# Optimization experiments

Measured on AMD Instinct MI355X. Metric: run time of the kernel, lower is better.

## Reference

```python
import jax, jax.numpy as jnp
import numpy as np


def setup_inputs() -> dict:
    key = jax.random.key(0)
    ks = jax.random.split(key, 9)
    N, K, CS, CT, OUT, S = 50000, 16, 64, 64, 64, 4
    x = jax.random.normal(ks[0], (N, CT), dtype=jnp.float32)
    src = jax.random.normal(ks[1], (N, CS), dtype=jnp.float32)
    neighbor_idx = jax.random.randint(ks[2], (N, K), 0, N, dtype=jnp.int32)
    scale_t = 1.0 / np.sqrt(CT)
    scale_s = 1.0 / np.sqrt(CS)
    Wt = jax.random.normal(ks[3], (CT, S), dtype=jnp.float32) * scale_t
    bt = jax.random.normal(ks[4], (S,), dtype=jnp.float32) * scale_t
    Ws = jax.random.normal(ks[5], (CS, S), dtype=jnp.float32) * scale_s
    bs = jax.random.normal(ks[6], (S,), dtype=jnp.float32) * scale_s
    W_lin = jax.random.normal(ks[7], (S, CS, OUT), dtype=jnp.float32) * scale_s
    b_lin = jax.random.normal(ks[8], (S, OUT), dtype=jnp.float32) * scale_s
    return {"x": x, "src": src, "neighbor_idx": neighbor_idx,
            "Wt": Wt, "bt": bt, "Ws": Ws, "bs": bs,
            "W_lin": W_lin, "b_lin": b_lin}


def reference(x, src, neighbor_idx, Wt, bt, Ws, bs, W_lin, b_lin):
    # Gather per-node neighbor messages: [N, K, Cs]
    msgs = src[neighbor_idx]
    size = Wt.shape[-1]
    # target assignment logits from own data: [N, S]
    t = x @ Wt + bt
    # source assignment logits from messages: [N, K, S]
    s = jnp.einsum('nkc,cs->nks', msgs, Ws) + bs
    # soft assignment over the `size` weight matrices (softmax over S)
    a = jax.nn.softmax(s + t[:, None, :], axis=-1)  # [N, K, S]
    # apply each of the `size` linears to the messages: [N, K, S, O]
    w = jnp.einsum('nkc,sco->nkso', msgs, W_lin) + b_lin
    # assignment-weighted mean over the S weight matrices: [N, K, O]
    out = jnp.einsum('nks,nkso->nko', a, w) / size
    return out
```

## Files before the change

kernel.cpp:

```cpp
#include <hip/hip_runtime.h>

#define CT 64
#define CS 64
#define K_NB 16
#define S_SZ 4
#define OUT_C 64
#define CAP 64
#define JB 4

typedef float vfloat4 __attribute__((ext_vector_type(4)));

__global__ __launch_bounds__(256) void kt_both(
    const float* __restrict__ x, const float* __restrict__ src,
    const float* __restrict__ Wt, const float* __restrict__ bt,
    const float* __restrict__ Ws, const float* __restrict__ bs,
    float* __restrict__ t_out, float* __restrict__ sl_out, int N)
{
    int gt = blockIdx.x * 256 + threadIdx.x;
    int r = gt >> 3, part = gt & 7;
    if (r >= N) return;
    const float4* xv = (const float4*)(x   + (size_t)r * 64) + part * 2;
    const float4* sv = (const float4*)(src + (size_t)r * 64) + part * 2;
    const float4* Wt4 = (const float4*)Wt;
    const float4* Ws4 = (const float4*)Ws;
    float4 xq0 = xv[0], xq1 = xv[1];
    float4 sq0 = sv[0], sq1 = sv[1];
    int c0 = part * 8;
    float4 at = {0.f, 0.f, 0.f, 0.f};
    float4 as = {0.f, 0.f, 0.f, 0.f};
    float xc[8] = {xq0.x, xq0.y, xq0.z, xq0.w, xq1.x, xq1.y, xq1.z, xq1.w};
    float sc[8] = {sq0.x, sq0.y, sq0.z, sq0.w, sq1.x, sq1.y, sq1.z, sq1.w};
    #pragma unroll
    for (int u = 0; u < 8; ++u) {
        float4 wt = Wt4[c0 + u];
        float4 ws = Ws4[c0 + u];
        at.x = fmaf(xc[u], wt.x, at.x);
        at.y = fmaf(xc[u], wt.y, at.y);
        at.z = fmaf(xc[u], wt.z, at.z);
        at.w = fmaf(xc[u], wt.w, at.w);
        as.x = fmaf(sc[u], ws.x, as.x);
        as.y = fmaf(sc[u], ws.y, as.y);
        as.z = fmaf(sc[u], ws.z, as.z);
        as.w = fmaf(sc[u], ws.w, as.w);
    }
    #pragma unroll
    for (int m = 1; m < 8; m <<= 1) {
        at.x += __shfl_xor(at.x, m); at.y += __shfl_xor(at.y, m);
        at.z += __shfl_xor(at.z, m); at.w += __shfl_xor(at.w, m);
        as.x += __shfl_xor(as.x, m); as.y += __shfl_xor(as.y, m);
        as.z += __shfl_xor(as.z, m); as.w += __shfl_xor(as.w, m);
    }
    if (part == 0) {
        float4 bbt = *(const float4*)bt;
        float4 bbs = *(const float4*)bs;
        at.x += bbt.x; at.y += bbt.y; at.z += bbt.z; at.w += bbt.w;
        as.x += bbs.x; as.y += bbs.y; as.z += bbs.z; as.w += bbs.w;
        ((float4*)t_out)[r]  = at;
        ((float4*)sl_out)[r] = as;
    }
}

__global__ __launch_bounds__(256) void kh_zero(int* __restrict__ cursor, int N)
{
    int i = blockIdx.x * 256 + threadIdx.x;
    if (i < N) cursor[i] = 0;
}

__global__ __launch_bounds__(256) void kh_fill_fixed(
    const int* __restrict__ nidx, int* __restrict__ cursor,
    int* __restrict__ plist, int NK)
{
    int p = blockIdx.x * 256 + threadIdx.x;
    if (p >= NK) return;
    int j = __builtin_nontemporal_load(nidx + p);
    int pos = atomicAdd(&cursor[j], 1);
    if (pos < CAP) plist[(size_t)j * CAP + pos] = p;
}

__global__ __launch_bounds__(256) void k_main(
    const int* __restrict__ cursor, const int* __restrict__ plist,
    const float* __restrict__ src,
    const float* __restrict__ W_lin, const float* __restrict__ b_lin,
    const float* __restrict__ t_in, const float* __restrict__ sl_in,
    float* __restrict__ out, int N)
{
    const int col = threadIdx.x;
    const int s = col >> 6, o = col & 63;
    float w[64];
    #pragma unroll
    for (int c = 0; c < 64; ++c)
        w[c] = W_lin[s * 4096 + (c << 6) + o];
    const float bl = b_lin[col];
    const int g = col >> 4;
    const int lane16 = col & 15;
    __shared__ float4 lsrc4[2][JB][16];
    __shared__ float4 zl4[2][JB][64];

    const int pstride = gridDim.x * JB;
    int jbase = blockIdx.x * JB;
    int b = 0;
    if (col < 16 * JB) {
        int jj = col >> 4, q = col & 15;
        int j0 = jbase + jj;
        if (j0 < N)
            lsrc4[0][jj][q] = ((const float4*)src)[((size_t)j0 << 4) + q];
    }
    __syncthreads();

    for (; jbase < N; jbase += pstride, b ^= 1) {
        #pragma unroll
        for (int jj = 0; jj < JB; ++jj) {
            float a0 = bl, a1 = 0.f, a2 = 0.f, a3 = 0.f;
            #pragma unroll
            for (int c4 = 0; c4 < 16; ++c4) {
                float4 s4 = lsrc4[b][jj][c4];
                a0 = fmaf(s4.x, w[c4 * 4 + 0], a0);
                a1 = fmaf(s4.y, w[c4 * 4 + 1], a1);
                a2 = fmaf(s4.z, w[c4 * 4 + 2], a2);
                a3 = fmaf(s4.w, w[c4 * 4 + 3], a3);
            }
            ((float*)zl4[b][jj])[col] = (a0 + a1) + (a2 + a3);
        }
        {
            int nb = jbase + pstride;
            if (col < 16 * JB) {
                int jj = col >> 4, q = col & 15;
                int j0 = nb + jj;
                if (j0 < N)
                    lsrc4[b ^ 1][jj][q] =
                        ((const float4*)src)[((size_t)j0 << 4) + q];
            }
        }
        int cnt[JB]; float4 slv[JB];
        #pragma unroll
        for (int jj = 0; jj < JB; ++jj) {
            int j = jbase + jj;
            if (j < N) {
                int c_ = cursor[j];
                cnt[jj] = c_ < CAP ? c_ : CAP;
                slv[jj] = ((const float4*)sl_in)[j];
            } else {
                cnt[jj] = 0;
                slv[jj] = make_float4(0.f, 0.f, 0.f, 0.f);
            }
        }
        __syncthreads();
        #pragma unroll
        for (int jj = 0; jj < JB; ++jj) {
            const int off = (jbase + jj) * CAP;
            const float4 sv = slv[jj];
            for (int ib = g; ib < cnt[jj]; ib += 16) {
                const int p = __builtin_nontemporal_load(plist + off + ib);
                const int n = p >> 4;
                float4 tv = ((const float4*)t_in)[n];
                float l0 = tv.x + sv.x, l1 = tv.y + sv.y;
                float l2 = tv.z + sv.z, l3 = tv.w + sv.w;
                float m = fmaxf(fmaxf(l0, l1), fmaxf(l2, l3));
                float e0 = __expf(l0 - m), e1 = __expf(l1 - m);
                float e2 = __expf(l2 - m), e3 = __expf(l3 - m);
                float inv = 0.25f / (e0 + e1 + e2 + e3);
                float4 z0 = zl4[b][jj][lane16];
                float4 z1 = zl4[b][jj][16 + lane16];
                float4 z2 = zl4[b][jj][32 + lane16];
                float4 z3 = zl4[b][jj][48 + lane16];
                vfloat4 ov;
                ov.x = (e0 * z0.x + e1 * z1.x + e2 * z2.x + e3 * z3.x) * inv;
                ov.y = (e0 * z0.y + e1 * z1.y + e2 * z2.y + e3 * z3.y) * inv;
                ov.z = (e0 * z0.z + e1 * z1.z + e2 * z2.z + e3 * z3.z) * inv;
                ov.w = (e0 * z0.w + e1 * z1.w + e2 * z2.w + e3 * z3.w) * inv;
                __builtin_nontemporal_store(
                    ov, (vfloat4*)out + (size_t)p * 16 + lane16);
            }
        }
    }
}

extern "C" void kernel_launch(void* const* d_in, const int* in_sizes, int n_in,
                              void* d_out, int out_size, void* d_ws, size_t ws_size,
                              hipStream_t stream)
{
    const float* x   = (const float*)d_in[0];
    const float* src = (const float*)d_in[1];
    const int*   idx = (const int*)d_in[2];
    const float* Wt  = (const float*)d_in[3];
    const float* bt  = (const float*)d_in[4];
    const float* Ws  = (const float*)d_in[5];
    const float* bs  = (const float*)d_in[6];
    const float* Wl  = (const float*)d_in[7];
    const float* bl  = (const float*)d_in[8];
    float* out = (float*)d_out;

    const int N  = in_sizes[0] / CT;
    const int NK = N * K_NB;

    float* t  = (float*)d_ws;
    float* sl = t + (size_t)N * 4;
    int* cursor = (int*)(sl + (size_t)N * 4);
    int* plist  = cursor + N;

    const int gbN   = (N + 255) / 256;
    const int gbNK  = (NK + 255) / 256;
    const int gbRow = (N * 8 + 255) / 256;
    const int gbMain = (N + (256 * JB) - 1) / (256 * JB) * 256 / 256;
    const int mainGrid = (N + JB * 4 - 1) / (JB * 4);
    (void)gbMain;

    hipLaunchKernelGGL(kh_zero, dim3(gbN), dim3(256), 0, stream, cursor, N);
    hipLaunchKernelGGL(kh_fill_fixed, dim3(gbNK), dim3(256), 0, stream,
                       idx, cursor, plist, NK);
    hipLaunchKernelGGL(kt_both, dim3(gbRow), dim3(256), 0, stream,
                       x, src, Wt, bt, Ws, bs, t, sl, N);
    hipLaunchKernelGGL(k_main, dim3(mainGrid), dim3(256), 0, stream,
                       cursor, plist, src, Wl, bl, t, sl, out, N);
}
```

Before: 379.5 us.

## Flatten neighbor loop across JB targets with prefetch, fuse cursor zeroing, vectorize fill

Zeroing the cursor array moves into the projection kernel, which removes one launch. The fill kernel now loads four indices per thread as a vector. k_main doubles JB to 8 and replaces the per-target loops with one flattened loop over all incoming entries, using prefix sums of the counts. It software-prefetches the next plist entry and t row, and stages the sl rows in shared memory. This aims to balance work across the 16 groups and hide gather latency, at the cost of more index arithmetic and registers.

New measurement: 374.2 us. No clear change (-1.4%).

```diff
diff --git a/kernel.cpp b/kernel.cpp
--- a/kernel.cpp
+++ b/kernel.cpp
@@ -6,17 +6,21 @@
 #define S_SZ 4
 #define OUT_C 64
 #define CAP 64
-#define JB 4
+#define JB 8
+#define PHASES 4
 
 typedef float vfloat4 __attribute__((ext_vector_type(4)));
+typedef int   vint4   __attribute__((ext_vector_type(4)));
 
 __global__ __launch_bounds__(256) void kt_both(
     const float* __restrict__ x, const float* __restrict__ src,
     const float* __restrict__ Wt, const float* __restrict__ bt,
     const float* __restrict__ Ws, const float* __restrict__ bs,
-    float* __restrict__ t_out, float* __restrict__ sl_out, int N)
+    float* __restrict__ t_out, float* __restrict__ sl_out,
+    int* __restrict__ cursor, int N)
 {
     int gt = blockIdx.x * 256 + threadIdx.x;
+    if (gt < N) cursor[gt] = 0;
     int r = gt >> 3, part = gt & 7;
     if (r >= N) return;
     const float4* xv = (const float4*)(x   + (size_t)r * 64) + part * 2;
@@ -60,21 +64,20 @@
     }
 }
 
-__global__ __launch_bounds__(256) void kh_zero(int* __restrict__ cursor, int N)
-{
-    int i = blockIdx.x * 256 + threadIdx.x;
-    if (i < N) cursor[i] = 0;
-}
-
 __global__ __launch_bounds__(256) void kh_fill_fixed(
     const int* __restrict__ nidx, int* __restrict__ cursor,
     int* __restrict__ plist, int NK)
 {
-    int p = blockIdx.x * 256 + threadIdx.x;
-    if (p >= NK) return;
-    int j = __builtin_nontemporal_load(nidx + p);
-    int pos = atomicAdd(&cursor[j], 1);
-    if (pos < CAP) plist[(size_t)j * CAP + pos] = p;
+    int q = blockIdx.x * 256 + threadIdx.x;
+    int p0 = q << 2;
+    if (p0 >= NK) return;
+    vint4 jv = __builtin_nontemporal_load((const vint4*)nidx + q);
+    #pragma unroll
+    for (int u = 0; u < 4; ++u) {
+        int j = jv[u];
+        int pos = atomicAdd(&cursor[j], 1);
+        if (pos < CAP) plist[(size_t)j * CAP + pos] = p0 + u;
+    }
 }
 
 __global__ __launch_bounds__(256) void k_main(
@@ -95,6 +98,7 @@
     const int lane16 = col & 15;
     __shared__ float4 lsrc4[2][JB][16];
     __shared__ float4 zl4[2][JB][64];
+    __shared__ float4 slv_l[2][JB];
 
     const int pstride = gridDim.x * JB;
     int jbase = blockIdx.x * JB;
@@ -131,46 +135,76 @@
                         ((const float4*)src)[((size_t)j0 << 4) + q];
             }
         }
-        int cnt[JB]; float4 slv[JB];
+        if (col < JB) {
+            int j0 = jbase + col;
+            slv_l[b][col] = (j0 < N) ? ((const float4*)sl_in)[j0]
+                                     : make_float4(0.f, 0.f, 0.f, 0.f);
+        }
+        int cA[JB];
         #pragma unroll
         for (int jj = 0; jj < JB; ++jj) {
-            int j = jbase + jj;
-            if (j < N) {
-                int c_ = cursor[j];
-                cnt[jj] = c_ < CAP ? c_ : CAP;
-                slv[jj] = ((const float4*)sl_in)[j];
-            } else {
-                cnt[jj] = 0;
-                slv[jj] = make_float4(0.f, 0.f, 0.f, 0.f);
+            int j0 = jbase + jj;
+            int c_ = (j0 < N) ? cursor[j0] : 0;
+            cA[jj] = c_ < CAP ? c_ : CAP;
+        }
+        const int m1 = cA[0],      m2 = m1 + cA[1], m3 = m2 + cA[2];
+        const int m4 = m3 + cA[3], m5 = m4 + cA[4], m6 = m5 + cA[5];
+        const int m7 = m6 + cA[6], m8 = m7 + cA[7];
+        __syncthreads();
+        const int total = m8;
+        const size_t pbase = (size_t)jbase * CAP;
+        int e = g;
+        int p_pre = 0;
+        float4 tv_pre = make_float4(0.f, 0.f, 0.f, 0.f);
+        if (e < total) {
+            int jj = (e >= m1) + (e >= m2) + (e >= m3) + (e >= m4)
+                   + (e >= m5) + (e >= m6) + (e >= m7);
+            int lo = 0;
+            lo = e >= m1 ? m1 : lo; lo = e >= m2 ? m2 : lo;
+            lo = e >= m3 ? m3 : lo; lo = e >= m4 ? m4 : lo;
+            lo = e >= m5 ? m5 : lo; lo = e >= m6 ? m6 : lo;
+            lo = e >= m7 ? m7 : lo;
+            p_pre = __builtin_nontemporal_load(
+                        plist + pbase + jj * CAP + (e - lo));
+            tv_pre = ((const float4*)t_in)[p_pre >> 4];
+        }
+        while (e < total) {
+            const int p_cur = p_pre;
+            const float4 tv = tv_pre;
+            const int jj = (e >= m1) + (e >= m2) + (e >= m3) + (e >= m4)
+                         + (e >= m5) + (e >= m6) + (e >= m7);
+            const int en = e + 16;
+            if (en < total) {
+                int jn = (en >= m1) + (en >= m2) + (en >= m3) + (en >= m4)
+                       + (en >= m5) + (en >= m6) + (en >= m7);
+                int lo = 0;
+                lo = en >= m1 ? m1 : lo; lo = en >= m2 ? m2 : lo;
+                lo = en >= m3 ? m3 : lo; lo = en >= m4 ? m4 : lo;
+                lo = en >= m5 ? m5 : lo; lo = en >= m6 ? m6 : lo;
+                lo = en >= m7 ? m7 : lo;
+                p_pre = __builtin_nontemporal_load(
+                            plist + pbase + jn * CAP + (en - lo));
+                tv_pre = ((const float4*)t_in)[p_pre >> 4];
             }
-        }
-        __syncthreads();
-        #pragma unroll
-        for (int jj = 0; jj < JB; ++jj) {
-            const int off = (jbase + jj) * CAP;
-            const float4 sv = slv[jj];
-            for (int ib = g; ib < cnt[jj]; ib += 16) {
-                const int p = __builtin_nontemporal_load(plist + off + ib);
-                const int n = p >> 4;
-                float4 tv = ((const float4*)t_in)[n];
-                float l0 = tv.x + sv.x, l1 = tv.y + sv.y;
-                float l2 = tv.z + sv.z, l3 = tv.w + sv.w;
-                float m = fmaxf(fmaxf(l0, l1), fmaxf(l2, l3));
-                float e0 = __expf(l0 - m), e1 = __expf(l1 - m);
-                float e2 = __expf(l2 - m), e3 = __expf(l3 - m);
-                float inv = 0.25f / (e0 + e1 + e2 + e3);
-                float4 z0 = zl4[b][jj][lane16];
-                float4 z1 = zl4[b][jj][16 + lane16];
-                float4 z2 = zl4[b][jj][32 + lane16];
-                float4 z3 = zl4[b][jj][48 + lane16];
-                vfloat4 ov;
-                ov.x = (e0 * z0.x + e1 * z1.x + e2 * z2.x + e3 * z3.x) * inv;
-                ov.y = (e0 * z0.y + e1 * z1.y + e2 * z2.y + e3 * z3.y) * inv;
-                ov.z = (e0 * z0.z + e1 * z1.z + e2 * z2.z + e3 * z3.z) * inv;
-                ov.w = (e0 * z0.w + e1 * z1.w + e2 * z2.w + e3 * z3.w) * inv;
-                __builtin_nontemporal_store(
-                    ov, (vfloat4*)out + (size_t)p * 16 + lane16);
-            }
+            const float4 sv = slv_l[b][jj];
+            float l0 = tv.x + sv.x, l1 = tv.y + sv.y;
+            float l2 = tv.z + sv.z, l3 = tv.w + sv.w;
+            float m = fmaxf(fmaxf(l0, l1), fmaxf(l2, l3));
+            float e0 = __expf(l0 - m), e1 = __expf(l1 - m);
+            float e2 = __expf(l2 - m), e3 = __expf(l3 - m);
+            float inv = 0.25f / (e0 + e1 + e2 + e3);
+            float4 z0 = zl4[b][jj][lane16];
+            float4 z1 = zl4[b][jj][16 + lane16];
+            float4 z2 = zl4[b][jj][32 + lane16];
+            float4 z3 = zl4[b][jj][48 + lane16];
+            vfloat4 ov;
+            ov.x = (e0 * z0.x + e1 * z1.x + e2 * z2.x + e3 * z3.x) * inv;
+            ov.y = (e0 * z0.y + e1 * z1.y + e2 * z2.y + e3 * z3.y) * inv;
+            ov.z = (e0 * z0.z + e1 * z1.z + e2 * z2.z + e3 * z3.z) * inv;
+            ov.w = (e0 * z0.w + e1 * z1.w + e2 * z2.w + e3 * z3.w) * inv;
+            __builtin_nontemporal_store(
+                ov, (vfloat4*)out + (size_t)p_cur * 16 + lane16);
+            e = en;
         }
     }
 }
@@ -198,18 +232,14 @@
     int* cursor = (int*)(sl + (size_t)N * 4);
     int* plist  = cursor + N;
 
-    const int gbN   = (N + 255) / 256;
-    const int gbNK  = (NK + 255) / 256;
-    const int gbRow = (N * 8 + 255) / 256;
-    const int gbMain = (N + (256 * JB) - 1) / (256 * JB) * 256 / 256;
-    const int mainGrid = (N + JB * 4 - 1) / (JB * 4);
-    (void)gbMain;
-
-    hipLaunchKernelGGL(kh_zero, dim3(gbN), dim3(256), 0, stream, cursor, N);
-    hipLaunchKernelGGL(kh_fill_fixed, dim3(gbNK), dim3(256), 0, stream,
+    const int gbRow  = (N * 8 + 255) / 256;
+    const int gbFill = (NK / 4 + 255) / 256;
+    const int mainGrid = (N + JB * PHASES - 1) / (JB * PHASES);
+
+    hipLaunchKernelGGL(kt_both, dim3(gbRow), dim3(256), 0, stream,
+                       x, src, Wt, bt, Ws, bs, t, sl, cursor, N);
+    hipLaunchKernelGGL(kh_fill_fixed, dim3(gbFill), dim3(256), 0, stream,
                        idx, cursor, plist, NK);
-    hipLaunchKernelGGL(kt_both, dim3(gbRow), dim3(256), 0, stream,
-                       x, src, Wt, bt, Ws, bs, t, sl, N);
     hipLaunchKernelGGL(k_main, dim3(mainGrid), dim3(256), 0, stream,
                        cursor, plist, src, Wl, bl, t, sl, out, N);
 }
```
